# Kernel optimization log

Measured on AMD Instinct MI355X. Metric: run time of the kernel, lower is better.

## Reference

```python
import jax, jax.numpy as jnp
import numpy as np

VOCAB = 1024
HIDDEN = 1024


def setup_inputs() -> dict:
    key = jax.random.key(0)
    k_x, k_wih, k_whh, k_bih, k_bhh = jax.random.split(key, 5)
    B, T = 32, 512
    bound = 1.0 / np.sqrt(HIDDEN)  # torch LSTMCell init: U(-1/sqrt(H), 1/sqrt(H))
    x = jax.random.normal(k_x, (B, T, VOCAB), dtype=jnp.float32)
    W_ih = jax.random.uniform(k_wih, (4 * HIDDEN, VOCAB), minval=-bound, maxval=bound, dtype=jnp.float32)
    W_hh = jax.random.uniform(k_whh, (4 * HIDDEN, HIDDEN), minval=-bound, maxval=bound, dtype=jnp.float32)
    b_ih = jax.random.uniform(k_bih, (4 * HIDDEN,), minval=-bound, maxval=bound, dtype=jnp.float32)
    b_hh = jax.random.uniform(k_bhh, (4 * HIDDEN,), minval=-bound, maxval=bound, dtype=jnp.float32)
    return {"x": x, "W_ih": W_ih, "W_hh": W_hh, "b_ih": b_ih, "b_hh": b_hh}


def _lstm_scan(x, W_ih, W_hh, b_ih, b_hh):
    B = x.shape[0]
    H = W_hh.shape[1]
    # Precompute input projections for all timesteps in one big GEMM: [B,T,4H]
    x_proj = jnp.einsum('btv,gv->btg', x, W_ih) + b_ih + b_hh

    def step(carry, xp_t):
        h, c = carry
        gates = xp_t + h @ W_hh.T  # [B, 4H]
        i, f, g, o = jnp.split(gates, 4, axis=-1)  # torch LSTMCell gate order
        i = jax.nn.sigmoid(i)
        f = jax.nn.sigmoid(f)
        g = jnp.tanh(g)
        o = jax.nn.sigmoid(o)
        c_new = f * c + i * g
        h_new = o * jnp.tanh(c_new)
        return (h_new, c_new), h_new

    h0 = jnp.zeros((B, H), dtype=x.dtype)
    c0 = jnp.zeros((B, H), dtype=x.dtype)
    # scan over time: x_proj transposed to [T, B, 4H]
    _, hs = jax.lax.scan(step, (h0, c0), jnp.swapaxes(x_proj, 0, 1))
    return jnp.swapaxes(hs, 0, 1)  # [B, T, H]


def reference(x, W_ih, W_hh, b_ih, b_hh):
    return _lstm_scan(x, W_ih, W_hh, b_ih, b_hh)
```

## Files before the change

### kernel.cpp

```cpp
#include <hip/hip_runtime.h>
#include <hip/hip_bf16.h>
#include <stdint.h>

#define HID 1024
#define VOC 1024
#define BB  32
#define TT  512
#define G4  4096
#define NBLK 128
#define POIS 0x7FC07FC0u

typedef float f32x4 __attribute__((ext_vector_type(4)));
typedef short bf16x8 __attribute__((ext_vector_type(8)));
typedef unsigned int u32x4 __attribute__((ext_vector_type(4)));

static __device__ __forceinline__ unsigned short f2bf(float f) {
    union { float f; unsigned u; } v; v.f = f;
    unsigned r = (v.u + 0x7FFFu + ((v.u >> 16) & 1u)) >> 16;
    return (unsigned short)r;
}
static __device__ __forceinline__ float bf2f(unsigned short s) {
    union { unsigned u; float f; } v; v.u = ((unsigned)s) << 16;
    return v.f;
}

__global__ void cvt_f32_bf16(const float* __restrict__ in,
                             unsigned short* __restrict__ out, int n4) {
    int i = blockIdx.x * blockDim.x + threadIdx.x;
    if (i >= n4) return;
    float4 v = ((const float4*)in)[i];
    ushort4 o;
    o.x = f2bf(v.x); o.y = f2bf(v.y); o.z = f2bf(v.z); o.w = f2bf(v.w);
    ((ushort4*)out)[i] = o;
}

__global__ void init_h(unsigned* __restrict__ h0, unsigned* __restrict__ h1,
                       unsigned* __restrict__ h2) {
    int i = blockIdx.x * 256 + threadIdx.x;
    if (i < BB * HID / 2) { h0[i] = 0u; h1[i] = POIS; h2[i] = POIS; }
}

__global__ __launch_bounds__(256) void gemm_xproj(
    const unsigned short* __restrict__ A, const unsigned short* __restrict__ W,
    const float* __restrict__ bih, const float* __restrict__ bhh,
    unsigned short* __restrict__ XP)
{
    __shared__ unsigned short As[128 * 64];
    __shared__ unsigned short Bs[128 * 64];
    const int tid  = threadIdx.x;
    const int lane = tid & 63;
    const int wid  = tid >> 6;
    const int mt = blockIdx.x & 127;
    const int nt = blockIdx.x >> 7;
    const long m0 = (long)mt * 128;
    const long n0 = (long)nt * 128;

    const int wr = wid >> 1, wc = wid & 1;
    const int rl = lane & 15;
    const int kl = (lane >> 4) * 8;

    f32x4 acc[4][4] = {};

    for (int kt = 0; kt < 16; ++kt) {
#pragma unroll
        for (int it = 0; it < 4; ++it) {
            int slot = it * 256 + tid;
            int r = slot >> 3, c8 = slot & 7;
            const unsigned short* ga = A + (m0 + r) * 1024 + kt * 64 + c8 * 8;
            const unsigned short* gb = W + (n0 + r) * 1024 + kt * 64 + c8 * 8;
            char* la = (char*)As + (it * 256 + wid * 64) * 16;
            char* lb = (char*)Bs + (it * 256 + wid * 64) * 16;
            __builtin_amdgcn_global_load_lds(
                (const __attribute__((address_space(1))) void*)ga,
                (__attribute__((address_space(3))) void*)la, 16, 0, 0);
            __builtin_amdgcn_global_load_lds(
                (const __attribute__((address_space(1))) void*)gb,
                (__attribute__((address_space(3))) void*)lb, 16, 0, 0);
        }
        __syncthreads();
#pragma unroll
        for (int kk = 0; kk < 2; ++kk) {
            bf16x8 af[4], bfr[4];
#pragma unroll
            for (int i = 0; i < 4; ++i) {
                int ar = wr * 64 + i * 16 + rl;
                int br = wc * 64 + i * 16 + rl;
                af[i]  = *(const bf16x8*)(As + ar * 64 + kk * 32 + kl);
                bfr[i] = *(const bf16x8*)(Bs + br * 64 + kk * 32 + kl);
            }
#pragma unroll
            for (int i = 0; i < 4; ++i)
#pragma unroll
                for (int j = 0; j < 4; ++j)
                    acc[i][j] = __builtin_amdgcn_mfma_f32_16x16x32_bf16(
                        af[i], bfr[j], acc[i][j], 0, 0, 0);
        }
        __syncthreads();
    }
#pragma unroll
    for (int i = 0; i < 4; ++i)
#pragma unroll
        for (int j = 0; j < 4; ++j)
#pragma unroll
            for (int r = 0; r < 4; ++r) {
                long row = m0 + wr * 64 + i * 16 + (lane >> 4) * 4 + r;
                long col = n0 + wc * 64 + j * 16 + (lane & 15);
                long orow = (row & 511) * 32 + (row >> 9);
                float v = acc[i][j][r] + bih[col] + bhh[col];
                XP[orow * 4096 + col] = f2bf(v);
            }
}

__global__ __launch_bounds__(512, 2) void lstm_scan(
    const unsigned short* __restrict__ Whh,
    const unsigned short* __restrict__ XP,
    unsigned* __restrict__ hb0,
    unsigned* __restrict__ hb1,
    unsigned* __restrict__ hb2,
    float* __restrict__ out)
{
    __shared__ float part[8][4][16][20];

    const int tid  = threadIdx.x;
    const int lane = tid & 63;
    const int kq   = tid >> 6;
    const int nl   = lane & 15;
    const int kh   = lane >> 4;
    const int jblk = blockIdx.x & 63;
    const int bh   = blockIdx.x >> 6;
    const int j0   = jblk * 16;

#define DECL_W(g) \
    const unsigned short* wb##g = Whh + (long)(g * 1024 + j0 + nl) * 1024 + kq * 128 + kh * 8; \
    bf16x8 w##g##0 = *(const bf16x8*)(wb##g +  0); \
    bf16x8 w##g##1 = *(const bf16x8*)(wb##g + 32); \
    bf16x8 w##g##2 = *(const bf16x8*)(wb##g + 64); \
    bf16x8 w##g##3 = *(const bf16x8*)(wb##g + 96);
    DECL_W(0) DECL_W(1) DECL_W(2) DECL_W(3)

    const long pOff = ((long)(bh * 16 + nl) * 1024 + kq * 128 + kh * 8) * 2;

    const bool act  = tid < 128;
    const int eb16  = tid >> 3;
    const int pu    = tid & 7;
    const int ju    = pu * 2;
    const int eb    = bh * 16 + eb16;
    const int hword = eb * 512 + jblk * 8 + pu;
    float creg0 = 0.f, creg1 = 0.f;

    const unsigned* XP32 = (const unsigned*)XP;
    unsigned xpr[4] = {};
    if (act) {
        const long xb = (long)eb * 2048 + jblk * 8 + pu;
        xpr[0] = XP32[xb];        xpr[1] = XP32[xb + 512];
        xpr[2] = XP32[xb + 1024]; xpr[3] = XP32[xb + 1536];
    }

    unsigned* rbuf = hb0; unsigned* wbuf = hb1; unsigned* pbuf = hb2;
    const unsigned pois = POIS;

    union CV { u32x4 u; bf16x8 v; };

    for (int t = 0; t < TT; ++t) {
        u32x4 f0, f1, f2, f3;
        {
            const char* rb = (const char*)rbuf + pOff;
            while (true) {
                asm volatile("global_load_dwordx4 %0, %1, off sc0 sc1"
                             : "=v"(f0) : "v"(rb) : "memory");
                asm volatile("global_load_dwordx4 %0, %1, off offset:64 sc0 sc1"
                             : "=v"(f1) : "v"(rb) : "memory");
                asm volatile("global_load_dwordx4 %0, %1, off offset:128 sc0 sc1"
                             : "=v"(f2) : "v"(rb) : "memory");
                asm volatile("global_load_dwordx4 %0, %1, off offset:192 sc0 sc1"
                             : "=v"(f3) : "v"(rb) : "memory");
                asm volatile("s_waitcnt vmcnt(0)" ::: "memory");
                int dirty = 0;
#pragma unroll
                for (int i = 0; i < 4; ++i)
                    dirty |= (f0[i] == POIS) | (f1[i] == POIS) |
                             (f2[i] == POIS) | (f3[i] == POIS);
                if (!__any(dirty)) break;
                __builtin_amdgcn_s_sleep(1);
            }
        }

        unsigned xpn[4] = {};
        if (act) {
            unsigned* pp = pbuf + hword;
            asm volatile("global_store_dword %0, %1, off sc0 sc1"
                         :: "v"(pp), "v"(pois) : "memory");
            const long tn = (t + 1 < TT) ? (t + 1) : t;
            const long xb = (tn * 32 + eb) * 2048 + jblk * 8 + pu;
            xpn[0] = XP32[xb];        xpn[1] = XP32[xb + 512];
            xpn[2] = XP32[xb + 1024]; xpn[3] = XP32[xb + 1536];
        }

        asm volatile("" : "+v"(w00), "+v"(w01), "+v"(w02), "+v"(w03),
                          "+v"(w10), "+v"(w11), "+v"(w12), "+v"(w13),
                          "+v"(w20), "+v"(w21), "+v"(w22), "+v"(w23),
                          "+v"(w30), "+v"(w31), "+v"(w32), "+v"(w33));
        f32x4 acc0 = {}, acc1 = {}, acc2 = {}, acc3 = {};
        {
            CV c0, c1, c2, c3;
            c0.u = f0; c1.u = f1; c2.u = f2; c3.u = f3;
            acc0 = __builtin_amdgcn_mfma_f32_16x16x32_bf16(c0.v, w00, acc0, 0, 0, 0);
            acc1 = __builtin_amdgcn_mfma_f32_16x16x32_bf16(c0.v, w10, acc1, 0, 0, 0);
            acc2 = __builtin_amdgcn_mfma_f32_16x16x32_bf16(c0.v, w20, acc2, 0, 0, 0);
            acc3 = __builtin_amdgcn_mfma_f32_16x16x32_bf16(c0.v, w30, acc3, 0, 0, 0);
            acc0 = __builtin_amdgcn_mfma_f32_16x16x32_bf16(c1.v, w01, acc0, 0, 0, 0);
            acc1 = __builtin_amdgcn_mfma_f32_16x16x32_bf16(c1.v, w11, acc1, 0, 0, 0);
            acc2 = __builtin_amdgcn_mfma_f32_16x16x32_bf16(c1.v, w21, acc2, 0, 0, 0);
            acc3 = __builtin_amdgcn_mfma_f32_16x16x32_bf16(c1.v, w31, acc3, 0, 0, 0);
            acc0 = __builtin_amdgcn_mfma_f32_16x16x32_bf16(c2.v, w02, acc0, 0, 0, 0);
            acc1 = __builtin_amdgcn_mfma_f32_16x16x32_bf16(c2.v, w12, acc1, 0, 0, 0);
            acc2 = __builtin_amdgcn_mfma_f32_16x16x32_bf16(c2.v, w22, acc2, 0, 0, 0);
            acc3 = __builtin_amdgcn_mfma_f32_16x16x32_bf16(c2.v, w32, acc3, 0, 0, 0);
            acc0 = __builtin_amdgcn_mfma_f32_16x16x32_bf16(c3.v, w03, acc0, 0, 0, 0);
            acc1 = __builtin_amdgcn_mfma_f32_16x16x32_bf16(c3.v, w13, acc1, 0, 0, 0);
            acc2 = __builtin_amdgcn_mfma_f32_16x16x32_bf16(c3.v, w23, acc2, 0, 0, 0);
            acc3 = __builtin_amdgcn_mfma_f32_16x16x32_bf16(c3.v, w33, acc3, 0, 0, 0);
        }

#pragma unroll
        for (int r = 0; r < 4; ++r) {
            part[kq][0][kh * 4 + r][nl] = acc0[r];
            part[kq][1][kh * 4 + r][nl] = acc1[r];
            part[kq][2][kh * 4 + r][nl] = acc2[r];
            part[kq][3][kh * 4 + r][nl] = acc3[r];
        }
        __syncthreads();

        float gv0[4], gv1[4];
        if (act) {
#pragma unroll
            for (int g = 0; g < 4; ++g) {
                float a0 = 0.f, a1 = 0.f;
#pragma unroll
                for (int q = 0; q < 8; ++q) {
                    const float2 p = *(const float2*)&part[q][g][eb16][ju];
                    a0 += p.x; a1 += p.y;
                }
                gv0[g] = a0 + bf2f((unsigned short)(xpr[g] & 0xffff));
                gv1[g] = a1 + bf2f((unsigned short)(xpr[g] >> 16));
            }
        }
        __syncthreads();

        if (act) {
            float i0 = 1.f / (1.f + __expf(-gv0[0]));
            float f0g = 1.f / (1.f + __expf(-gv0[1]));
            float g0 = tanhf(gv0[2]);
            float o0 = 1.f / (1.f + __expf(-gv0[3]));
            creg0 = f0g * creg0 + i0 * g0;
            float hn0 = o0 * tanhf(creg0);
            float i1 = 1.f / (1.f + __expf(-gv1[0]));
            float f1g = 1.f / (1.f + __expf(-gv1[1]));
            float g1 = tanhf(gv1[2]);
            float o1 = 1.f / (1.f + __expf(-gv1[3]));
            creg1 = f1g * creg1 + i1 * g1;
            float hn1 = o1 * tanhf(creg1);

            unsigned hv = (unsigned)f2bf(hn0) | ((unsigned)f2bf(hn1) << 16);
            unsigned* wp = wbuf + hword;
            asm volatile("global_store_dword %0, %1, off sc0 sc1"
                         :: "v"(wp), "v"(hv) : "memory");

            float2 ov; ov.x = hn0; ov.y = hn1;
            *(float2*)&out[((long)eb * TT + t) * HID + j0 + ju] = ov;
#pragma unroll
            for (int g = 0; g < 4; ++g) xpr[g] = xpn[g];
        }

        unsigned* tmp = rbuf; rbuf = wbuf; wbuf = pbuf; pbuf = tmp;
    }
}

extern "C" void kernel_launch(void* const* d_in, const int* in_sizes, int n_in,
                              void* d_out, int out_size, void* d_ws, size_t ws_size,
                              hipStream_t stream)
{
    const float* x   = (const float*)d_in[0];
    const float* Wih = (const float*)d_in[1];
    const float* Whh = (const float*)d_in[2];
    const float* bih = (const float*)d_in[3];
    const float* bhh = (const float*)d_in[4];
    float* out = (float*)d_out;

    char* ws = (char*)d_ws;
    size_t off = 0;
    auto alloc = [&](size_t bytes) {
        char* p = ws + off;
        off = (off + bytes + 255) & ~(size_t)255;
        return p;
    };
    unsigned short* x_bf   = (unsigned short*)alloc((size_t)BB * TT * VOC * 2);
    unsigned short* wih_bf = (unsigned short*)alloc((size_t)G4 * VOC * 2);
    unsigned short* whh_bf = (unsigned short*)alloc((size_t)G4 * HID * 2);
    unsigned short* xp     = (unsigned short*)alloc((size_t)TT * BB * G4 * 2);
    unsigned* hb0          = (unsigned*)alloc((size_t)BB * HID * 2);
    unsigned* hb1          = (unsigned*)alloc((size_t)BB * HID * 2);
    unsigned* hb2          = (unsigned*)alloc((size_t)BB * HID * 2);

    int n4x = BB * TT * VOC / 4;
    cvt_f32_bf16<<<(n4x + 255) / 256, 256, 0, stream>>>(x, x_bf, n4x);
    int n4w = G4 * VOC / 4;
    cvt_f32_bf16<<<(n4w + 255) / 256, 256, 0, stream>>>(Wih, wih_bf, n4w);
    cvt_f32_bf16<<<(n4w + 255) / 256, 256, 0, stream>>>(Whh, whh_bf, n4w);

    gemm_xproj<<<4096, 256, 0, stream>>>(x_bf, wih_bf, bih, bhh, xp);

    init_h<<<64, 256, 0, stream>>>(hb0, hb1, hb2);

    lstm_scan<<<NBLK, 512, 0, stream>>>(whh_bf, xp, hb0, hb1, hb2, out);
}
```

Before: 2.849 ms.

## Move half of recurrent weights to swizzled LDS and double-buffer partial sums

Half of each block's W_hh slice (the g and o gates) now lives in XOR-swizzled shared memory instead of registers, so each thread holds fewer VGPRs. The partial-sum buffer is double-buffered by timestep parity, which removes the second __syncthreads per step. The spin-wait now retries only the poisoned h chunks with a longer sleep, and the next-step XP prefetch moves after the gate math. The cost is eight extra LDS reads per step on the critical path and roughly 64KB of LDS per block, which may limit blocks per CU under the launch bound of 2.

```diff
diff --git a/kernel.cpp b/kernel.cpp
--- a/kernel.cpp
+++ b/kernel.cpp
@@ -22,6 +22,9 @@
 static __device__ __forceinline__ float bf2f(unsigned short s) {
     union { unsigned u; float f; } v; v.u = ((unsigned)s) << 16;
     return v.f;
+}
+static __device__ __forceinline__ int vd(u32x4 v) {
+    return (v[0] == POIS) | (v[1] == POIS) | (v[2] == POIS) | (v[3] == POIS);
 }
 
 __global__ void cvt_f32_bf16(const float* __restrict__ in,
@@ -119,7 +122,8 @@
     unsigned* __restrict__ hb2,
     float* __restrict__ out)
 {
-    __shared__ float part[8][4][16][20];
+    __shared__ unsigned short Wlds[32 * 1024];
+    __shared__ float part[2][8][4][16][18];
 
     const int tid  = threadIdx.x;
     const int lane = tid & 63;
@@ -130,15 +134,25 @@
     const int bh   = blockIdx.x >> 6;
     const int j0   = jblk * 16;
 
-#define DECL_W(g) \
-    const unsigned short* wb##g = Whh + (long)(g * 1024 + j0 + nl) * 1024 + kq * 128 + kh * 8; \
-    bf16x8 w##g##0 = *(const bf16x8*)(wb##g +  0); \
-    bf16x8 w##g##1 = *(const bf16x8*)(wb##g + 32); \
-    bf16x8 w##g##2 = *(const bf16x8*)(wb##g + 64); \
-    bf16x8 w##g##3 = *(const bf16x8*)(wb##g + 96);
-    DECL_W(0) DECL_W(1) DECL_W(2) DECL_W(3)
+    for (int i = 0; i < 8; ++i) {
+        int g16 = tid + i * 512;
+        int rn  = g16 >> 7;
+        int kc  = g16 & 127;
+        bf16x8 v = *(const bf16x8*)(Whh +
+            (long)((2 + (rn >> 4)) * 1024 + j0 + (rn & 15)) * 1024 + kc * 8);
+        *(bf16x8*)((char*)Wlds + ((rn * 2048 + kc * 16) ^ ((rn & 7) << 4))) = v;
+    }
+
+    const unsigned short* wbi = Whh + (long)(j0 + nl) * 1024 + kq * 128 + kh * 8;
+    const unsigned short* wbf = Whh + (long)(1024 + j0 + nl) * 1024 + kq * 128 + kh * 8;
+    bf16x8 wi0 = *(const bf16x8*)(wbi +  0), wi1 = *(const bf16x8*)(wbi + 32),
+           wi2 = *(const bf16x8*)(wbi + 64), wi3 = *(const bf16x8*)(wbi + 96);
+    bf16x8 wf0 = *(const bf16x8*)(wbf +  0), wf1 = *(const bf16x8*)(wbf + 32),
+           wf2 = *(const bf16x8*)(wbf + 64), wf3 = *(const bf16x8*)(wbf + 96);
 
     const long pOff = ((long)(bh * 16 + nl) * 1024 + kq * 128 + kh * 8) * 2;
+    const int  swzx = (nl & 7) << 4;
+    const int  kb   = (kq * 128 + kh * 8) * 2;
 
     const bool act  = tid < 128;
     const int eb16  = tid >> 3;
@@ -161,93 +175,105 @@
 
     union CV { u32x4 u; bf16x8 v; };
 
+    __syncthreads();
+
     for (int t = 0; t < TT; ++t) {
+        const int tb = t & 1;
+
         u32x4 f0, f1, f2, f3;
         {
             const char* rb = (const char*)rbuf + pOff;
-            while (true) {
-                asm volatile("global_load_dwordx4 %0, %1, off sc0 sc1"
-                             : "=v"(f0) : "v"(rb) : "memory");
-                asm volatile("global_load_dwordx4 %0, %1, off offset:64 sc0 sc1"
-                             : "=v"(f1) : "v"(rb) : "memory");
-                asm volatile("global_load_dwordx4 %0, %1, off offset:128 sc0 sc1"
-                             : "=v"(f2) : "v"(rb) : "memory");
-                asm volatile("global_load_dwordx4 %0, %1, off offset:192 sc0 sc1"
-                             : "=v"(f3) : "v"(rb) : "memory");
+            asm volatile("global_load_dwordx4 %0, %1, off sc0 sc1"
+                         : "=v"(f0) : "v"(rb) : "memory");
+            asm volatile("global_load_dwordx4 %0, %1, off offset:64 sc0 sc1"
+                         : "=v"(f1) : "v"(rb) : "memory");
+            asm volatile("global_load_dwordx4 %0, %1, off offset:128 sc0 sc1"
+                         : "=v"(f2) : "v"(rb) : "memory");
+            asm volatile("global_load_dwordx4 %0, %1, off offset:192 sc0 sc1"
+                         : "=v"(f3) : "v"(rb) : "memory");
+            asm volatile("s_waitcnt vmcnt(0)" ::: "memory");
+            __builtin_amdgcn_sched_barrier(0);
+            int d0 = vd(f0), d1 = vd(f1), d2 = vd(f2), d3 = vd(f3);
+            while (__any(d0 | d1 | d2 | d3)) {
+                __builtin_amdgcn_s_sleep(2);
+                if (d0) asm volatile("global_load_dwordx4 %0, %1, off sc0 sc1"
+                                     : "=v"(f0) : "v"(rb) : "memory");
+                if (d1) asm volatile("global_load_dwordx4 %0, %1, off offset:64 sc0 sc1"
+                                     : "=v"(f1) : "v"(rb) : "memory");
+                if (d2) asm volatile("global_load_dwordx4 %0, %1, off offset:128 sc0 sc1"
+                                     : "=v"(f2) : "v"(rb) : "memory");
+                if (d3) asm volatile("global_load_dwordx4 %0, %1, off offset:192 sc0 sc1"
+                                     : "=v"(f3) : "v"(rb) : "memory");
                 asm volatile("s_waitcnt vmcnt(0)" ::: "memory");
-                int dirty = 0;
-#pragma unroll
-                for (int i = 0; i < 4; ++i)
-                    dirty |= (f0[i] == POIS) | (f1[i] == POIS) |
-                             (f2[i] == POIS) | (f3[i] == POIS);
-                if (!__any(dirty)) break;
-                __builtin_amdgcn_s_sleep(1);
+                __builtin_amdgcn_sched_barrier(0);
+                if (d0) d0 = vd(f0);
+                if (d1) d1 = vd(f1);
+                if (d2) d2 = vd(f2);
+                if (d3) d3 = vd(f3);
             }
         }
 
-        unsigned xpn[4] = {};
         if (act) {
             unsigned* pp = pbuf + hword;
             asm volatile("global_store_dword %0, %1, off sc0 sc1"
                          :: "v"(pp), "v"(pois) : "memory");
-            const long tn = (t + 1 < TT) ? (t + 1) : t;
-            const long xb = (tn * 32 + eb) * 2048 + jblk * 8 + pu;
-            xpn[0] = XP32[xb];        xpn[1] = XP32[xb + 512];
-            xpn[2] = XP32[xb + 1024]; xpn[3] = XP32[xb + 1536];
-        }
-
-        asm volatile("" : "+v"(w00), "+v"(w01), "+v"(w02), "+v"(w03),
-                          "+v"(w10), "+v"(w11), "+v"(w12), "+v"(w13),
-                          "+v"(w20), "+v"(w21), "+v"(w22), "+v"(w23),
-                          "+v"(w30), "+v"(w31), "+v"(w32), "+v"(w33));
+        }
+
+        asm volatile("" : "+v"(wi0), "+v"(wi1), "+v"(wi2), "+v"(wi3),
+                          "+v"(wf0), "+v"(wf1), "+v"(wf2), "+v"(wf3));
         f32x4 acc0 = {}, acc1 = {}, acc2 = {}, acc3 = {};
         {
             CV c0, c1, c2, c3;
             c0.u = f0; c1.u = f1; c2.u = f2; c3.u = f3;
-            acc0 = __builtin_amdgcn_mfma_f32_16x16x32_bf16(c0.v, w00, acc0, 0, 0, 0);
-            acc1 = __builtin_amdgcn_mfma_f32_16x16x32_bf16(c0.v, w10, acc1, 0, 0, 0);
-            acc2 = __builtin_amdgcn_mfma_f32_16x16x32_bf16(c0.v, w20, acc2, 0, 0, 0);
-            acc3 = __builtin_amdgcn_mfma_f32_16x16x32_bf16(c0.v, w30, acc3, 0, 0, 0);
-            acc0 = __builtin_amdgcn_mfma_f32_16x16x32_bf16(c1.v, w01, acc0, 0, 0, 0);
-            acc1 = __builtin_amdgcn_mfma_f32_16x16x32_bf16(c1.v, w11, acc1, 0, 0, 0);
-            acc2 = __builtin_amdgcn_mfma_f32_16x16x32_bf16(c1.v, w21, acc2, 0, 0, 0);
-            acc3 = __builtin_amdgcn_mfma_f32_16x16x32_bf16(c1.v, w31, acc3, 0, 0, 0);
-            acc0 = __builtin_amdgcn_mfma_f32_16x16x32_bf16(c2.v, w02, acc0, 0, 0, 0);
-            acc1 = __builtin_amdgcn_mfma_f32_16x16x32_bf16(c2.v, w12, acc1, 0, 0, 0);
-            acc2 = __builtin_amdgcn_mfma_f32_16x16x32_bf16(c2.v, w22, acc2, 0, 0, 0);
-            acc3 = __builtin_amdgcn_mfma_f32_16x16x32_bf16(c2.v, w32, acc3, 0, 0, 0);
-            acc0 = __builtin_amdgcn_mfma_f32_16x16x32_bf16(c3.v, w03, acc0, 0, 0, 0);
-            acc1 = __builtin_amdgcn_mfma_f32_16x16x32_bf16(c3.v, w13, acc1, 0, 0, 0);
-            acc2 = __builtin_amdgcn_mfma_f32_16x16x32_bf16(c3.v, w23, acc2, 0, 0, 0);
-            acc3 = __builtin_amdgcn_mfma_f32_16x16x32_bf16(c3.v, w33, acc3, 0, 0, 0);
+            const char* wl = (const char*)Wlds;
+            bf16x8 wg0 = *(const bf16x8*)(wl + ((nl * 2048 + kb +   0) ^ swzx));
+            bf16x8 wg1 = *(const bf16x8*)(wl + ((nl * 2048 + kb +  64) ^ swzx));
+            bf16x8 wg2 = *(const bf16x8*)(wl + ((nl * 2048 + kb + 128) ^ swzx));
+            bf16x8 wg3 = *(const bf16x8*)(wl + ((nl * 2048 + kb + 192) ^ swzx));
+            bf16x8 wo0 = *(const bf16x8*)(wl + 32768 + ((nl * 2048 + kb +   0) ^ swzx));
+            bf16x8 wo1 = *(const bf16x8*)(wl + 32768 + ((nl * 2048 + kb +  64) ^ swzx));
+            bf16x8 wo2 = *(const bf16x8*)(wl + 32768 + ((nl * 2048 + kb + 128) ^ swzx));
+            bf16x8 wo3 = *(const bf16x8*)(wl + 32768 + ((nl * 2048 + kb + 192) ^ swzx));
+            acc0 = __builtin_amdgcn_mfma_f32_16x16x32_bf16(c0.v, wi0, acc0, 0, 0, 0);
+            acc1 = __builtin_amdgcn_mfma_f32_16x16x32_bf16(c0.v, wf0, acc1, 0, 0, 0);
+            acc0 = __builtin_amdgcn_mfma_f32_16x16x32_bf16(c1.v, wi1, acc0, 0, 0, 0);
+            acc1 = __builtin_amdgcn_mfma_f32_16x16x32_bf16(c1.v, wf1, acc1, 0, 0, 0);
+            acc0 = __builtin_amdgcn_mfma_f32_16x16x32_bf16(c2.v, wi2, acc0, 0, 0, 0);
+            acc1 = __builtin_amdgcn_mfma_f32_16x16x32_bf16(c2.v, wf2, acc1, 0, 0, 0);
+            acc0 = __builtin_amdgcn_mfma_f32_16x16x32_bf16(c3.v, wi3, acc0, 0, 0, 0);
+            acc1 = __builtin_amdgcn_mfma_f32_16x16x32_bf16(c3.v, wf3, acc1, 0, 0, 0);
+            acc2 = __builtin_amdgcn_mfma_f32_16x16x32_bf16(c0.v, wg0, acc2, 0, 0, 0);
+            acc3 = __builtin_amdgcn_mfma_f32_16x16x32_bf16(c0.v, wo0, acc3, 0, 0, 0);
+            acc2 = __builtin_amdgcn_mfma_f32_16x16x32_bf16(c1.v, wg1, acc2, 0, 0, 0);
+            acc3 = __builtin_amdgcn_mfma_f32_16x16x32_bf16(c1.v, wo1, acc3, 0, 0, 0);
+            acc2 = __builtin_amdgcn_mfma_f32_16x16x32_bf16(c2.v, wg2, acc2, 0, 0, 0);
+            acc3 = __builtin_amdgcn_mfma_f32_16x16x32_bf16(c2.v, wo2, acc3, 0, 0, 0);
+            acc2 = __builtin_amdgcn_mfma_f32_16x16x32_bf16(c3.v, wg3, acc2, 0, 0, 0);
+            acc3 = __builtin_amdgcn_mfma_f32_16x16x32_bf16(c3.v, wo3, acc3, 0, 0, 0);
         }
 
 #pragma unroll
         for (int r = 0; r < 4; ++r) {
-            part[kq][0][kh * 4 + r][nl] = acc0[r];
-            part[kq][1][kh * 4 + r][nl] = acc1[r];
-            part[kq][2][kh * 4 + r][nl] = acc2[r];
-            part[kq][3][kh * 4 + r][nl] = acc3[r];
+            part[tb][kq][0][kh * 4 + r][nl] = acc0[r];
+            part[tb][kq][1][kh * 4 + r][nl] = acc1[r];
+            part[tb][kq][2][kh * 4 + r][nl] = acc2[r];
+            part[tb][kq][3][kh * 4 + r][nl] = acc3[r];
         }
         __syncthreads();
 
-        float gv0[4], gv1[4];
         if (act) {
+            float gv0[4], gv1[4];
 #pragma unroll
             for (int g = 0; g < 4; ++g) {
                 float a0 = 0.f, a1 = 0.f;
 #pragma unroll
                 for (int q = 0; q < 8; ++q) {
-                    const float2 p = *(const float2*)&part[q][g][eb16][ju];
+                    const float2 p = *(const float2*)&part[tb][q][g][eb16][ju];
                     a0 += p.x; a1 += p.y;
                 }
                 gv0[g] = a0 + bf2f((unsigned short)(xpr[g] & 0xffff));
                 gv1[g] = a1 + bf2f((unsigned short)(xpr[g] >> 16));
             }
-        }
-        __syncthreads();
-
-        if (act) {
             float i0 = 1.f / (1.f + __expf(-gv0[0]));
             float f0g = 1.f / (1.f + __expf(-gv0[1]));
             float g0 = tanhf(gv0[2]);
@@ -268,8 +294,10 @@
 
             float2 ov; ov.x = hn0; ov.y = hn1;
             *(float2*)&out[((long)eb * TT + t) * HID + j0 + ju] = ov;
-#pragma unroll
-            for (int g = 0; g < 4; ++g) xpr[g] = xpn[g];
+            const long tn = (t + 1 < TT) ? (t + 1) : t;
+            const long xb = (tn * 32 + eb) * 2048 + jblk * 8 + pu;
+            xpr[0] = XP32[xb];        xpr[1] = XP32[xb + 512];
+            xpr[2] = XP32[xb + 1024]; xpr[3] = XP32[xb + 1536];
         }
 
         unsigned* tmp = rbuf; rbuf = wbuf; wbuf = pbuf; pbuf = tmp;
```

Result: faster. 2.715 ms (-4.7%).
